# Kernel tuning notes

Hardware: AMD Instinct MI355X
Metric: run time of the kernel (lower is better)

The kernel has to match this reference:

```python
import jax, jax.numpy as jnp
import numpy as np

H = 256          # node_hidden_size (hardcoded in __init__)
NODE_EMB = 128   # node_emb_size
EDGE_EMB = 64    # edge_emb_size
L_EXTRA = 3      # num_layers - 1
NODE_FEATS = (40, 6, 5)
EDGE_FEATS = (5, 4)
T = 16           # max_seq_length
B = 32           # batch
LATENT = 128


def _lstm(inp, h, c, Wi, Wh, bi, bh):
    g = inp @ Wi + bi + h @ Wh + bh
    i, f, gg, o = jnp.split(g, 4, axis=-1)  # torch LSTMCell gate order
    c2 = jax.nn.sigmoid(f) * c + jax.nn.sigmoid(i) * jnp.tanh(gg)
    h2 = jax.nn.sigmoid(o) * jnp.tanh(c2)
    return h2, c2


def _cell(x, ctx, hs, cs, p):
    # DecoderCell: context concatenated to input of first layer, stack of LSTM cells,
    # linear projection of top hidden to emb.
    Wi0, Wh0, bi0, bh0, Wis, Whs, bis, bhs, Wout, bout = p
    inp = jnp.concatenate([x, ctx], axis=-1)
    h, c = _lstm(inp, hs[0], cs[0], Wi0, Wh0, bi0, bh0)
    nh, nc = [h], [c]
    for l in range(L_EXTRA):
        h, c = _lstm(h, hs[l + 1], cs[l + 1], Wis[l], Whs[l], bis[l], bhs[l])
        nh.append(h); nc.append(c)
    emb = h @ Wout + bout
    return emb, jnp.stack(nh), jnp.stack(nc)


def _ce(logits, tgt):
    # F.cross_entropy(..., ignore_index=-1), mean over valid batch entries
    valid = tgt >= 0
    t = jnp.where(valid, tgt, 0)
    logp = jax.nn.log_softmax(logits, axis=-1)
    nll = -jnp.take_along_axis(logp, t[:, None], axis=-1)[:, 0]
    n = jnp.sum(valid)
    return jnp.sum(jnp.where(valid, nll, 0.0)) / jnp.maximum(n, 1)


def _loss(z, latent_W, latent_b, node_p, edge_p, ncls, ecls, atom_target, bond_target):
    ctx = z @ latent_W + latent_b  # [B, H]
    NL = 1 + L_EXTRA
    hs0 = jnp.zeros((NL, B, H), jnp.float32)
    cs0 = jnp.zeros((NL, B, H), jnp.float32)
    buf0 = jnp.zeros((T, B, NODE_EMB), jnp.float32)
    x0 = jnp.zeros((B, H), jnp.float32)

    def node_step(carry, i):
        hs, cs, x, buf, loss = carry
        emb, hs2, cs2 = _cell(x, ctx, hs, cs, node_p)  # node_cell(x)
        for k, (W, b) in enumerate(ncls):
            loss = loss + _ce(emb @ W + b, atom_target[i, :, k])
        buf2 = buf.at[i].set(emb)
        ectx = cs2[-1]  # node_cell.hidden[-1][1]
        ehs0 = jnp.zeros((NL, B, H), jnp.float32)
        ecs0 = jnp.zeros((NL, B, H), jnp.float32)

        def edge_step(ec, j):
            ehs, ecs, eloss = ec
            eemb, ehs2, ecs2 = _cell(buf2[j], ectx, ehs, ecs, edge_p)
            valid = j < i  # only previous node embeddings exist; padding masked out
            ehs2 = jnp.where(valid, ehs2, ehs)
            ecs2 = jnp.where(valid, ecs2, ecs)
            for k, (W, b) in enumerate(ecls):
                eloss = eloss + _ce(eemb @ W + b, bond_target[i, :, j, k])
            return (ehs2, ecs2, eloss), None

        # reversed(node_embeddings): process j = T-1 .. 0; invalid prefix keeps zero hidden
        (ehs, ecs, eloss), _ = jax.lax.scan(
            edge_step, (ehs0, ecs0, jnp.float32(0.0)), jnp.arange(T - 1, -1, -1))
        xn = ecs[-1]  # x = edge_cell.hidden[-1][1]
        return (hs2, cs2, xn, buf2, loss + eloss), None

    init = (hs0, cs0, x0, buf0, jnp.float32(0.0))
    (hs, cs, x, buf, loss), _ = jax.lax.scan(node_step, init, jnp.arange(T))
    return loss


def setup_inputs() -> dict:
    key = jax.random.key(0)
    ks = iter(jax.random.split(key, 64))
    def rn(shape, s=0.05):
        return (jax.random.normal(next(ks), shape) * s).astype(jnp.float32)
    H4 = 4 * H
    inp = {
        'z': rn((B, LATENT), 1.0),
        'latent_W': rn((LATENT, H)), 'latent_b': rn((H,)),
        'nWi0': rn((2 * H, H4)), 'nWh0': rn((H, H4)), 'nbi0': rn((H4,)), 'nbh0': rn((H4,)),
        'nWi': rn((L_EXTRA, H, H4)), 'nWh': rn((L_EXTRA, H, H4)),
        'nbi': rn((L_EXTRA, H4)), 'nbh': rn((L_EXTRA, H4)),
        'nOutW': rn((H, NODE_EMB)), 'nOutb': rn((NODE_EMB,)),
        'eWi0': rn((NODE_EMB + H, H4)), 'eWh0': rn((H, H4)), 'ebi0': rn((H4,)), 'ebh0': rn((H4,)),
        'eWi': rn((L_EXTRA, H, H4)), 'eWh': rn((L_EXTRA, H, H4)),
        'ebi': rn((L_EXTRA, H4)), 'ebh': rn((L_EXTRA, H4)),
        'eOutW': rn((H, EDGE_EMB)), 'eOutb': rn((EDGE_EMB,)),
        'ncW0': rn((NODE_EMB, NODE_FEATS[0])), 'ncb0': rn((NODE_FEATS[0],)),
        'ncW1': rn((NODE_EMB, NODE_FEATS[1])), 'ncb1': rn((NODE_FEATS[1],)),
        'ncW2': rn((NODE_EMB, NODE_FEATS[2])), 'ncb2': rn((NODE_FEATS[2],)),
        'ecW0': rn((EDGE_EMB, EDGE_FEATS[0])), 'ecb0': rn((EDGE_FEATS[0],)),
        'ecW1': rn((EDGE_EMB, EDGE_FEATS[1])), 'ecb1': rn((EDGE_FEATS[1],)),
    }
    rng = np.random.default_rng(0)
    at = np.stack([rng.integers(0, f, size=(T, B)) for f in NODE_FEATS], axis=-1).astype(np.int32)
    bt = np.stack([rng.integers(0, f, size=(T, B, T)) for f in EDGE_FEATS], axis=-1).astype(np.int32)
    for i in range(T):
        bt[i, :, i:, :] = -1  # no edges to non-existent previous nodes (ignore_index)
    inp['atom_target'] = jnp.asarray(at)
    inp['bond_target'] = jnp.asarray(bt)
    return inp


def reference(z, atom_target, bond_target, latent_W, latent_b,
              nWi0, nWh0, nbi0, nbh0, nWi, nWh, nbi, nbh, nOutW, nOutb,
              eWi0, eWh0, ebi0, ebh0, eWi, eWh, ebi, ebh, eOutW, eOutb,
              ncW0, ncb0, ncW1, ncb1, ncW2, ncb2, ecW0, ecb0, ecW1, ecb1):
    node_p = (nWi0, nWh0, nbi0, nbh0, nWi, nWh, nbi, nbh, nOutW, nOutb)
    edge_p = (eWi0, eWh0, ebi0, ebh0, eWi, eWh, ebi, ebh, eOutW, eOutb)
    ncls = ((ncW0, ncb0), (ncW1, ncb1), (ncW2, ncb2))
    ecls = ((ecW0, ecb0), (ecW1, ecb1))
    return _loss(z, latent_W, latent_b, node_p, edge_p, ncls, ecls, atom_target, bond_target)
```

## Files before the change

### kernel.cpp

```cpp
#include <hip/hip_runtime.h>
#include <stdint.h>


#define DEVFN __device__ __forceinline__
#define SCOPE __HIP_MEMORY_SCOPE_AGENT

typedef __attribute__((ext_vector_type(8))) short bf16x8;
typedef __attribute__((ext_vector_type(4))) float f32x4;

constexpr size_t O_FLAGS = 0;
constexpr size_t O_MISC  = 16384;
constexpr size_t O_CTX   = O_MISC + 256;
constexpr size_t O_CTXG  = O_CTX + 16384;
constexpr size_t O_ZBUF  = O_CTXG + 131072;
constexpr size_t O_XBUF  = O_ZBUF + 16384;
constexpr size_t O_ECTX  = O_XBUF + 16384;
constexpr size_t O_HN    = O_ECTX + 16384;
constexpr size_t O_HE    = O_HN + 8*16384;
constexpr size_t O_EMB   = O_HE + 6*16384;
constexpr size_t O_EH3   = O_EMB + 16*8192;
constexpr size_t O_WN0   = O_EH3 + 120*16384;
constexpr size_t O_WN0C  = O_WN0 + 1024*512*2;
constexpr size_t O_WN1   = O_WN0C + 1024*256*2;
constexpr size_t O_WE0   = O_WN1 + 3*1024*512*2;
constexpr size_t O_WE1   = O_WE0 + 1024*640*2;
constexpr size_t O_NOUT  = O_WE1 + 3*1024*512*2;
constexpr size_t O_EOUT  = O_NOUT + 128*256*2;
constexpr size_t O_BN0   = O_EOUT + 64*256*2;
constexpr size_t O_BN1   = O_BN0 + 4096;
constexpr size_t O_BE0   = O_BN1 + 3*4096;
constexpr size_t O_BE1   = O_BE0 + 4096;

struct GP {
  const float *z,*lW,*lb;
  const float *nWi0,*nWh0,*nbi0,*nbh0,*nWi,*nWh,*nbi,*nbh,*nOutW,*nOutb;
  const float *eWi0,*eWh0,*ebi0,*ebh0,*eWi,*eWh,*ebi,*ebh,*eOutW,*eOutb;
  const float *ncW0,*ncb0,*ncW1,*ncb1,*ncW2,*ncb2,*ecW0,*ecb0,*ecW1,*ecb1;
  const int *atom,*bond;
  float* out; char* ws;
};

DEVFN uint16_t f2bf(float f){
  uint32_t u=__float_as_uint(f);
  uint32_t r=u+0x7fffu+((u>>16)&1u);
  return (uint16_t)(r>>16);
}
DEVFN float bf2f(uint16_t h){ return __uint_as_float(((uint32_t)h)<<16); }
DEVFN uint64_t ald64(const void* p){ return __hip_atomic_load((const uint64_t*)p,__ATOMIC_RELAXED,SCOPE); }
DEVFN uint32_t ald32(const void* p){ return __hip_atomic_load((const uint32_t*)p,__ATOMIC_RELAXED,SCOPE); }
DEVFN void ast32(void* p, uint32_t v){ __hip_atomic_store((uint32_t*)p,v,__ATOMIC_RELAXED,SCOPE); }
DEVFN float sigm(float x){ return 1.f/(1.f+__expf(-x)); }
DEVFN void acq_fence(){ __builtin_amdgcn_fence(__ATOMIC_ACQUIRE, "agent"); }

template<int K0,int K1,int K2>
DEVFN f32x4 stage_mm3(const uint16_t* p0,const uint16_t* p1,const uint16_t* p2,
                      const uint16_t* W,int rowbase,int mtile,int ntile,int lane){
  constexpr int NK=(K0+K1+K2)/32;
  const int m=lane&15, quad=lane>>4;
  const uint16_t* wrow = W + (size_t)(rowbase+ntile*16+m)*(size_t)(K0+K1+K2);
  bf16x8 aq[NK], bq[NK];
  #pragma unroll
  for(int ks=0;ks<NK;ks++){
    const int kg=ks*32;
    const uint16_t* ap; int kl;
    if (kg < K0){ ap = p0 + (size_t)(mtile*16+m)*K0; kl = kg; }
    else if (kg < K0+K1){ ap = p1 + (size_t)(mtile*16+m)*K1; kl = kg-K0; }
    else { ap = p2 + (size_t)(mtile*16+m)*K2; kl = kg-K0-K1; }
    aq[ks]=*(const bf16x8*)(ap + kl + quad*8);
    bq[ks]=*(const bf16x8*)(wrow + kg + quad*8);
  }
  f32x4 acc={0.f,0.f,0.f,0.f};
  #pragma unroll
  for(int ks=0;ks<NK;ks++)
    acc=__builtin_amdgcn_mfma_f32_16x16x32_bf16(aq[ks],bq[ks],acc,0,0,0);
  return acc;
}

DEVFN void lstm_tail(float* lds,uint16_t* hout,float& creg,bool creset,
                     uint16_t* cexp,int wgl,int tid){
  __syncthreads();
  const int b=tid>>3, ul=tid&7;
  const float* gp=&lds[b*36+ul*4];
  float gi=gp[0],gf=gp[1],gg=gp[2],go=gp[3];
  float c = creset?0.f:creg;
  float c2 = sigm(gf)*c + sigm(gi)*tanhf(gg);
  float h2 = sigm(go)*tanhf(c2);
  creg=c2;
  float hp=__shfl_xor(h2,1);
  if(!(tid&1))
    ast32(hout + b*256 + wgl*8 + ul, (uint32_t)f2bf(h2)|(((uint32_t)f2bf(hp))<<16));
  if (cexp){
    float cp=__shfl_xor(c2,1);
    if(!(tid&1))
      ast32(cexp + b*256 + wgl*8 + ul, (uint32_t)f2bf(c2)|(((uint32_t)f2bf(cp))<<16));
  }
}

DEVFN void do_lstm_r(const uint16_t* p0,const uint16_t* p1,const bf16x8* wreg,
                     const float* bvec,const float* ctxg,
                     uint16_t* hout,float& creg,bool creset,uint16_t* cexp,
                     float* lds,int wgl,int tid){
  const int lane=tid&63, wv=tid>>6, mtile=wv&1, ntile=wv>>1;
  const int m=lane&15, quad=lane>>4;
  bf16x8 aq[16];
  #pragma unroll
  for(int ks=0;ks<16;ks++){
    const uint16_t* ap = (ks<8) ? p0 + (size_t)(mtile*16+m)*256 + ks*32
                                : p1 + (size_t)(mtile*16+m)*256 + (ks-8)*32;
    aq[ks]=*(const bf16x8*)(ap + quad*8);
  }
  f32x4 acc={0.f,0.f,0.f,0.f};
  #pragma unroll
  for(int ks=0;ks<16;ks++)
    acc=__builtin_amdgcn_mfma_f32_16x16x32_bf16(aq[ks],wreg[ks],acc,0,0,0);
  const int colL=ntile*16+m, colG=wgl*32+colL;
  float bias = bvec ? bvec[colG] : 0.f;
  #pragma unroll
  for(int r=0;r<4;r++){
    int b=mtile*16+quad*4+r;
    float v=acc[r]+bias;
    if (ctxg) v += ctxg[b*1024+colG];
    lds[b*36+colL]=v;
  }
  lstm_tail(lds,hout,creg,creset,cexp,wgl,tid);
}

template<int K0,int K1,int K2>
DEVFN void do_lstm_l(const uint16_t* p0,const uint16_t* p1,const uint16_t* p2,
                     const uint16_t* slab,const float* bvec,
                     uint16_t* hout,float& creg,bool creset,uint16_t* cexp,
                     float* lds,int wgl,int tid){
  constexpr int K=K0+K1+K2, KP=K+8, NK=K/32;
  const int lane=tid&63, wv=tid>>6, mtile=wv&1, ntile=wv>>1;
  const int m=lane&15, quad=lane>>4;
  bf16x8 aq[NK];
  #pragma unroll
  for(int ks=0;ks<NK;ks++){
    const int kg=ks*32;
    const uint16_t* ap; int kl;
    if (kg < K0){ ap = p0 + (size_t)(mtile*16+m)*K0; kl = kg; }
    else if (kg < K0+K1){ ap = p1 + (size_t)(mtile*16+m)*K1; kl = kg-K0; }
    else { ap = p2 + (size_t)(mtile*16+m)*K2; kl = kg-K0-K1; }
    aq[ks]=*(const bf16x8*)(ap + kl + quad*8);
  }
  const uint16_t* wrow = slab + (size_t)(ntile*16+m)*KP;
  f32x4 acc={0.f,0.f,0.f,0.f};
  #pragma unroll
  for(int ks=0;ks<NK;ks++){
    bf16x8 bv=*(const bf16x8*)(wrow + ks*32 + quad*8);
    acc=__builtin_amdgcn_mfma_f32_16x16x32_bf16(aq[ks],bv,acc,0,0,0);
  }
  const int colL=ntile*16+m, colG=wgl*32+colL;
  float bias=bvec[colG];
  #pragma unroll
  for(int r=0;r<4;r++){
    int b=mtile*16+quad*4+r;
    lds[b*36+colL]=acc[r]+bias;
  }
  lstm_tail(lds,hout,creg,creset,cexp,wgl,tid);
}

DEVFN void do_emb(const uint16_t* h3,const uint16_t* NOUT,const float* nOutb,
                  uint16_t* dst,int wg,int tid){
  const int lane=tid&63, wv=tid>>6;
  if (wg>=8 || wv>=2) return;
  f32x4 acc=stage_mm3<256,0,0>(h3,nullptr,nullptr,NOUT,wg*16,wv,0,lane);
  const int n=lane&15, quad=lane>>4, colG=wg*16+n;
  float bias=nOutb[colG];
  #pragma unroll
  for(int r=0;r<4;r++){
    int b=wv*16+quad*4+r;
    float v=acc[r]+bias;
    float vp=__shfl_xor(v,1);
    if(!(lane&1))
      ast32(dst + b*128 + colG, (uint32_t)f2bf(v)|(((uint32_t)f2bf(vp))<<16));
  }
}

DEVFN void node_ce(const GP& P,const uint16_t* emb,int i,float* sm,float& lsum,int tid){
  {
    int e=tid*16;
    const uint64_t* src=(const uint64_t*)(emb+e);
    int b=e>>7, k=e&127;
    #pragma unroll
    for(int q=0;q<4;q++){
      uint64_t w=ald64(src+q);
      #pragma unroll
      for(int x=0;x<4;x++) sm[b*132+k+q*4+x]=bf2f((uint16_t)(w>>(16*x)));
    }
  }
  __syncthreads();
  float* ll = sm + 4224;
  const float* Ws[3]={P.ncW0,P.ncW1,P.ncW2};
  const float* bs[3]={P.ncb0,P.ncb1,P.ncb2};
  const int NCs[3]={40,6,5};
  for(int h=0;h<3;h++){
    const int Nc=NCs[h]; const float* W=Ws[h]; const float* bb=bs[h];
    for(int idx=tid; idx<32*Nc; idx+=256){
      int b=idx/Nc, c=idx-b*Nc;
      float a=bb[c];
      for(int k=0;k<128;k++) a += sm[b*132+k]*W[k*Nc+c];
      ll[b*44+c]=a;
    }
    __syncthreads();
    if (tid<32){
      int b=tid; float mx=-1e30f;
      for(int c=0;c<Nc;c++) mx=fmaxf(mx,ll[b*44+c]);
      float se=0.f;
      for(int c=0;c<Nc;c++) se+=__expf(ll[b*44+c]-mx);
      float lse=mx+__logf(se);
      int tgt=P.atom[(i*32+b)*3+h];
      lsum += (lse - ll[b*44+tgt])*(1.0f/32.0f);
    }
    __syncthreads();
  }
}

DEVFN void edge_ce(const GP& P,const uint16_t* eh3,const uint16_t* EOUT,
                   int i,int j,float* sm,float& lsum,int tid){
  const int lane=tid&63, wv=tid>>6;
  float* el=sm; float* ll=sm+4224;
  #pragma unroll
  for(int t2=0;t2<2;t2++){
    int id=wv+4*t2, mtile=id>>2, ntile=id&3;
    f32x4 acc=stage_mm3<256,0,0>(eh3,nullptr,nullptr,EOUT,0,mtile,ntile,lane);
    int n=lane&15, quad=lane>>4, colG=ntile*16+n;
    float bias=P.eOutb[colG];
    #pragma unroll
    for(int r=0;r<4;r++){ int b=mtile*16+quad*4+r; el[b*68+colG]=acc[r]+bias; }
  }
  __syncthreads();
  const float* Ws[2]={P.ecW0,P.ecW1};
  const float* bs[2]={P.ecb0,P.ecb1};
  const int NCs[2]={5,4};
  for(int h=0;h<2;h++){
    const int Nc=NCs[h]; const float* W=Ws[h];
    for(int idx=tid; idx<32*Nc; idx+=256){
      int b=idx/Nc, c=idx-b*Nc;
      float a=bs[h][c];
      for(int k=0;k<64;k++) a += el[b*68+k]*W[k*Nc+c];
      ll[b*44+c]=a;
    }
    __syncthreads();
    if (tid<32){
      int b=tid; float mx=-1e30f;
      for(int c=0;c<Nc;c++) mx=fmaxf(mx,ll[b*44+c]);
      float se=0.f;
      for(int c=0;c<Nc;c++) se+=__expf(ll[b*44+c]-mx);
      float lse=mx+__logf(se);
      int tgt=P.bond[((i*32+b)*16+j)*2+h];
      lsum += (lse - ll[b*44+tgt])*(1.0f/32.0f);
    }
    __syncthreads();
  }
}

DEVFN void wg_spin(const uint32_t* flags,int s,int lane){
  const uint32_t* f1 = flags + (size_t)lane*32;
  const uint32_t* f2 = flags + (size_t)(lane+64)*32;
  while(true){
    uint32_t a=__hip_atomic_load(f1,__ATOMIC_RELAXED,SCOPE);
    uint32_t b=__hip_atomic_load(f2,__ATOMIC_RELAXED,SCOPE);
    if (__all(((int)a>=s) && ((int)b>=s))) break;
    __builtin_amdgcn_s_sleep(1);
  }
}

__global__ __launch_bounds__(256,1) void gen_prep(GP P){
  char* ws=P.ws;
  const int tid=threadIdx.x, wg=blockIdx.x, nwg=gridDim.x;
  if (wg==0){
    for(int n=tid;n<1024;n+=256){
      int col=(n&3)*256+(n>>2);
      ((float*)(ws+O_BN0))[n]=P.nbi0[col]+P.nbh0[col];
      ((float*)(ws+O_BE0))[n]=P.ebi0[col]+P.ebh0[col];
      for(int l=0;l<3;l++){
        ((float*)(ws+O_BN1))[l*1024+n]=P.nbi[l*1024+col]+P.nbh[l*1024+col];
        ((float*)(ws+O_BE1))[l*1024+n]=P.ebi[l*1024+col]+P.ebh[l*1024+col];
      }
    }
  } else if (wg==1){
    uint16_t* ctx=(uint16_t*)(ws+O_CTX);
    for(int idx=tid; idx<8192; idx+=256){
      int b=idx>>8, n=idx&255;
      float a=P.lb[n];
      for(int k=0;k<128;k++) a += P.z[b*128+k]*P.lW[k*256+n];
      ctx[idx]=f2bf(a);
    }
  } else if (wg==2){
    uint32_t* f=(uint32_t*)(ws+O_FLAGS);
    for(int idx=tid; idx<4096; idx+=256) f[idx]=0;
    if (tid<64) ((uint32_t*)(ws+O_MISC))[tid]=0;
  } else if (wg==3){
    uint32_t* zz=(uint32_t*)(ws+O_ZBUF);
    for(int idx=tid; idx<8192; idx+=256) zz[idx]=0;
  }
  const int ROWS=9408;
  int per=(ROWS+nwg-1)/nwg;
  int r0=wg*per, r1=(r0+per<ROWS)?(r0+per):ROWS;
  for(int r=r0;r<r1;r++){
    if (r<1024){
      int n=r, col=(n&3)*256+(n>>2);
      uint16_t* dst=(uint16_t*)(ws+O_WN0)+(size_t)n*512;
      for(int k=tid;k<512;k+=256)
        dst[k]=f2bf(k<256 ? P.nWi0[k*1024+col] : P.nWh0[(k-256)*1024+col]);
    } else if (r<2048){
      int n=r-1024, col=(n&3)*256+(n>>2);
      uint16_t* dst=(uint16_t*)(ws+O_WN0C)+(size_t)n*256;
      for(int k=tid;k<256;k+=256) dst[k]=f2bf(P.nWi0[(256+k)*1024+col]);
    } else if (r<5120){
      int t=r-2048, l=t>>10, n=t&1023, col=(n&3)*256+(n>>2);
      uint16_t* dst=(uint16_t*)(ws+O_WN1)+((size_t)l*1024+n)*512;
      for(int k=tid;k<512;k+=256)
        dst[k]=f2bf(k<256 ? P.nWi[(l*256+k)*1024+col] : P.nWh[(l*256+k-256)*1024+col]);
    } else if (r<6144){
      int n=r-5120, col=(n&3)*256+(n>>2);
      uint16_t* dst=(uint16_t*)(ws+O_WE0)+(size_t)n*640;
      for(int k=tid;k<640;k+=256)
        dst[k]=f2bf(k<384 ? P.eWi0[k*1024+col] : P.eWh0[(k-384)*1024+col]);
    } else if (r<9216){
      int t=r-6144, l=t>>10, n=t&1023, col=(n&3)*256+(n>>2);
      uint16_t* dst=(uint16_t*)(ws+O_WE1)+((size_t)l*1024+n)*512;
      for(int k=tid;k<512;k+=256)
        dst[k]=f2bf(k<256 ? P.eWi[(l*256+k)*1024+col] : P.eWh[(l*256+k-256)*1024+col]);
    } else if (r<9344){
      int n=r-9216;
      uint16_t* dst=(uint16_t*)(ws+O_NOUT)+(size_t)n*256;
      for(int k=tid;k<256;k+=256) dst[k]=f2bf(P.nOutW[k*128+n]);
    } else {
      int n=r-9344;
      uint16_t* dst=(uint16_t*)(ws+O_EOUT)+(size_t)n*256;
      for(int k=tid;k<256;k+=256) dst[k]=f2bf(P.eOutW[k*64+n]);
    }
  }
}

__global__ __launch_bounds__(256,1) void gen_main(GP P){
  __shared__ alignas(16) char smem[46080];
  char* ws=P.ws;
  uint32_t* flags=(uint32_t*)(ws+O_FLAGS);
  const int tid=threadIdx.x, wg=blockIdx.x, lane=tid&63;

  if (wg<128){
    uint16_t* slab=(uint16_t*)smem;
    float* gates=(float*)(smem+41472);
    uint16_t* WN0 =(uint16_t*)(ws+O_WN0);
    uint16_t* WN0C=(uint16_t*)(ws+O_WN0C);
    uint16_t* WN1 =(uint16_t*)(ws+O_WN1);
    uint16_t* NOUT=(uint16_t*)(ws+O_NOUT);
    const float* BN0 =(const float*)(ws+O_BN0);
    const float* BN1v=(const float*)(ws+O_BN1);
    const float* BE0v=(const float*)(ws+O_BE0);
    const float* BE1v=(const float*)(ws+O_BE1);
    float* ctxg=(float*)(ws+O_CTXG);
    uint16_t* xb=(uint16_t*)(ws+O_XBUF);
    uint16_t* ec=(uint16_t*)(ws+O_ECTX);
    const uint16_t* zb=(const uint16_t*)(ws+O_ZBUF);
    uint16_t* embw=(uint16_t*)(ws+O_EMB);
    uint16_t* eh3w=(uint16_t*)(ws+O_EH3);
    auto HN=[&](int l,int pp){ return (uint16_t*)(ws+O_HN)+(size_t)(l*2+pp)*8192; };
    auto HE=[&](int l,int pp){ return (uint16_t*)(ws+O_HE)+(size_t)(l*2+pp)*8192; };

    const int g=wg>>5, wgl=wg&31;

    {
      const int KW=(g==0)?640:512, CH=KW/8, KP=KW+8;
      const uint16_t* wsrc = (g==0)
        ? (const uint16_t*)(ws+O_WE0) + (size_t)(wgl*32)*640
        : (const uint16_t*)(ws+O_WE1) + ((size_t)((g-1)*1024 + wgl*32))*512;
      for(int c=tid; c<32*CH; c+=256){
        int r=c/CH, off=c-r*CH;
        *(uint4*)(slab + (size_t)r*KP + off*8) = *(const uint4*)(wsrc + (size_t)r*KW + off*8);
      }
    }
    bf16x8 wn[16];
    {
      const uint16_t* nsrc = (g==0) ? WN0 : WN1 + (size_t)(g-1)*1024*512;
      const int m=lane&15, quad=lane>>4, ntile=(tid>>6)>>1;
      const size_t row=(size_t)(wgl*32 + ntile*16 + m);
      #pragma unroll
      for(int ks=0;ks<16;ks++)
        wn[ks]=*(const bf16x8*)(nsrc + row*512 + ks*32 + quad*8);
    }

    auto bar=[&](int sv){
      __syncthreads();
      if (tid==0) ast32(flags+(size_t)wg*32,(uint32_t)sv);
      if (tid<64){ acq_fence(); wg_spin(flags,sv,lane); }
      __syncthreads();
    };

    int s=0;
    if (g==0){
      const int wv=tid>>6, mtile=wv&1, ntile=wv>>1;
      f32x4 acc=stage_mm3<256,0,0>((const uint16_t*)(ws+O_CTX),nullptr,nullptr,
                                   WN0C,wgl*32,mtile,ntile,lane);
      const int n=lane&15, quad=lane>>4, colG=wgl*32+ntile*16+n;
      float bias=BN0[colG];
      #pragma unroll
      for(int r=0;r<4;r++){
        int b=mtile*16+quad*4+r;
        ast32(&ctxg[b*1024+colG], __float_as_uint(acc[r]+bias));
      }
    }
    bar(++s);

    float cn=0.f;
    float ce=0.f;
    for(int i=0;i<16;i++){
      const int p=i&1;
      if (g==0) do_lstm_r(xb, i?HN(0,p^1):zb, wn, nullptr, ctxg,
                          HN(0,p), cn, i==0, nullptr, gates, wgl, tid);
      bar(++s);
      if (g==1) do_lstm_r(HN(0,p), i?HN(1,p^1):zb, wn, BN1v, nullptr,
                          HN(1,p), cn, i==0, nullptr, gates, wgl, tid);
      bar(++s);
      if (g==2) do_lstm_r(HN(1,p), i?HN(2,p^1):zb, wn, BN1v+1024, nullptr,
                          HN(2,p), cn, i==0, nullptr, gates, wgl, tid);
      bar(++s);
      if (g==3) do_lstm_r(HN(2,p), i?HN(3,p^1):zb, wn, BN1v+2048, nullptr,
                          HN(3,p), cn, i==0, ec, gates, wgl, tid);
      bar(++s);
      const int nslots=(i==0)?1:(i+3);
      for(int t=0;t<nslots;t++){
        if (g==1 && t==0){
          if (wgl<8) do_emb(HN(3,p), NOUT, P.nOutb, embw+(size_t)i*4096, wgl, tid);
        } else {
          const int q=t-g;
          if (q>=0 && q<=i-1){
            const int e=q&1, j=i-1-q, pos=(i*(i-1))/2+q;
            if (g==0)
              do_lstm_l<128,256,256>(embw+(size_t)j*4096, ec, q?HE(0,e^1):zb,
                                     slab, BE0v, HE(0,e), ce, q==0, nullptr, gates, wgl, tid);
            else if (g==1)
              do_lstm_l<256,256,0>(HE(0,e), q?HE(1,e^1):zb, nullptr,
                                   slab, BE1v, HE(1,e), ce, q==0, nullptr, gates, wgl, tid);
            else if (g==2)
              do_lstm_l<256,256,0>(HE(1,e), q?HE(2,e^1):zb, nullptr,
                                   slab, BE1v+1024, HE(2,e), ce, q==0, nullptr, gates, wgl, tid);
            else
              do_lstm_l<256,256,0>(HE(2,e), q?(eh3w+(size_t)(pos-1)*8192):zb, nullptr,
                                   slab, BE1v+2048, eh3w+(size_t)pos*8192, ce, q==0,
                                   (j==0)?xb:nullptr, gates, wgl, tid);
          }
        }
        bar(++s);
      }
    }
    if (wg==0 && tid==0){
      const uint32_t* dp=(const uint32_t*)(ws+O_MISC+4);
      while (__hip_atomic_load(dp,__ATOMIC_RELAXED,SCOPE) < 8u)
        __builtin_amdgcn_s_sleep(8);
      P.out[0]=__uint_as_float(ald32(ws+O_MISC));
    }
  } else {
    float* sm=(float*)smem;
    const int my=wg-128;
    float lsum=0.f;
    int task=0, sb=1;
    const uint16_t* embw=(const uint16_t*)(ws+O_EMB);
    const uint16_t* eh3w=(const uint16_t*)(ws+O_EH3);
    const uint16_t* EOUT=(const uint16_t*)(ws+O_EOUT);
    for(int i=0;i<16;i++){
      const int base=sb+4;
      if ((task++&7)==my){
        if (tid<64) wg_spin(flags, base+1, lane);
        __syncthreads();
        acq_fence();
        node_ce(P, embw+(size_t)i*4096, i, sm, lsum, tid);
      }
      for(int j=i-1;j>=0;j--){
        const int q=i-1-j;
        if ((task++&7)==my){
          if (tid<64) wg_spin(flags, base+q+4, lane);
          __syncthreads();
          acq_fence();
          const int pos=(i*(i-1))/2+q;
          edge_ce(P, eh3w+(size_t)pos*8192, EOUT, i, j, sm, lsum, tid);
        }
      }
      sb = base + ((i==0)?1:(i+3));
    }
    #pragma unroll
    for(int off=32;off;off>>=1) lsum += __shfl_down(lsum,off);
    __syncthreads();
    if ((tid&63)==0) sm[tid>>6]=lsum;
    __syncthreads();
    if (tid==0){
      float tt=sm[0]+sm[1]+sm[2]+sm[3];
      atomicAdd((float*)(ws+O_MISC), tt);
      __threadfence();
      atomicAdd((unsigned int*)(ws+O_MISC+4), 1u);
    }
  }
}

extern "C" void kernel_launch(void* const* d_in, const int* in_sizes, int n_in,
                              void* d_out, int out_size, void* d_ws, size_t ws_size,
                              hipStream_t stream){
  (void)in_sizes; (void)n_in; (void)out_size; (void)ws_size;
  GP P;
  P.z   =(const float*)d_in[0];  P.lW  =(const float*)d_in[1];  P.lb  =(const float*)d_in[2];
  P.nWi0=(const float*)d_in[3];  P.nWh0=(const float*)d_in[4];
  P.nbi0=(const float*)d_in[5];  P.nbh0=(const float*)d_in[6];
  P.nWi =(const float*)d_in[7];  P.nWh =(const float*)d_in[8];
  P.nbi =(const float*)d_in[9];  P.nbh =(const float*)d_in[10];
  P.nOutW=(const float*)d_in[11]; P.nOutb=(const float*)d_in[12];
  P.eWi0=(const float*)d_in[13]; P.eWh0=(const float*)d_in[14];
  P.ebi0=(const float*)d_in[15]; P.ebh0=(const float*)d_in[16];
  P.eWi =(const float*)d_in[17]; P.eWh =(const float*)d_in[18];
  P.ebi =(const float*)d_in[19]; P.ebh =(const float*)d_in[20];
  P.eOutW=(const float*)d_in[21]; P.eOutb=(const float*)d_in[22];
  P.ncW0=(const float*)d_in[23]; P.ncb0=(const float*)d_in[24];
  P.ncW1=(const float*)d_in[25]; P.ncb1=(const float*)d_in[26];
  P.ncW2=(const float*)d_in[27]; P.ncb2=(const float*)d_in[28];
  P.ecW0=(const float*)d_in[29]; P.ecb0=(const float*)d_in[30];
  P.ecW1=(const float*)d_in[31]; P.ecb1=(const float*)d_in[32];
  P.atom=(const int*)d_in[33];   P.bond=(const int*)d_in[34];
  P.out=(float*)d_out; P.ws=(char*)d_ws;
  hipLaunchKernelGGL(gen_prep, dim3(120), dim3(256), 0, stream, P);
  hipLaunchKernelGGL(gen_main, dim3(136), dim3(256), 0, stream, P);
}
```

Baseline: 1.173 ms.

## Tile weight conversion through LDS transpose with coalesced loads and stores

The prep kernel's per-row weight conversion, which read fp32 weights with strided column accesses, is replaced by 64x64 tiles. Each tile is read with coalesced float4 loads, converted to bf16, transposed through shared memory and written as 16-byte vector stores. The latent-context matmul is split across four workgroups instead of one, and the prep grid is doubled. This targets the uncoalesced global traffic and serial ctx computation in the one-time weight preparation, at the cost of two barriers per tile and more complex index mapping.

After: 1.058 ms (median of 2 runs). 9.8% less time.

```diff
diff --git a/kernel.cpp b/kernel.cpp
--- a/kernel.cpp
+++ b/kernel.cpp
@@ -266,7 +266,46 @@
   }
 }
 
+DEVFN void tile_desc(const GP& P, char* ws, int tile,
+                     uint16_t*& dst,int& L,int& koff,const float*& src,
+                     int& sstr,int& N0,bool& perm){
+  if (tile<1120){
+    perm=true; sstr=1024;
+    int kt=tile>>4; N0=(tile&15)*64;
+    if (kt<4){ dst=(uint16_t*)(ws+O_WN0); L=512; koff=kt*64;
+               src=P.nWi0 + (size_t)kt*64*1024; }
+    else if (kt<8){ int r=kt-4; dst=(uint16_t*)(ws+O_WN0); L=512; koff=256+r*64;
+               src=P.nWh0 + (size_t)r*64*1024; }
+    else if (kt<12){ int r=kt-8; dst=(uint16_t*)(ws+O_WN0C); L=256; koff=r*64;
+               src=P.nWi0 + (size_t)(256+r*64)*1024; }
+    else if (kt<24){ int t=kt-12,l=t>>2,r=t&3;
+               dst=(uint16_t*)(ws+O_WN1)+(size_t)l*1024*512; L=512; koff=r*64;
+               src=P.nWi + (size_t)(l*256+r*64)*1024; }
+    else if (kt<36){ int t=kt-24,l=t>>2,r=t&3;
+               dst=(uint16_t*)(ws+O_WN1)+(size_t)l*1024*512; L=512; koff=256+r*64;
+               src=P.nWh + (size_t)(l*256+r*64)*1024; }
+    else if (kt<42){ int r=kt-36; dst=(uint16_t*)(ws+O_WE0); L=640; koff=r*64;
+               src=P.eWi0 + (size_t)r*64*1024; }
+    else if (kt<46){ int r=kt-42; dst=(uint16_t*)(ws+O_WE0); L=640; koff=384+r*64;
+               src=P.eWh0 + (size_t)r*64*1024; }
+    else if (kt<58){ int t=kt-46,l=t>>2,r=t&3;
+               dst=(uint16_t*)(ws+O_WE1)+(size_t)l*1024*512; L=512; koff=r*64;
+               src=P.eWi + (size_t)(l*256+r*64)*1024; }
+    else { int t=kt-58,l=t>>2,r=t&3;
+               dst=(uint16_t*)(ws+O_WE1)+(size_t)l*1024*512; L=512; koff=256+r*64;
+               src=P.eWh + (size_t)(l*256+r*64)*1024; }
+  } else {
+    perm=false;
+    int t2=tile-1120;
+    if (t2<8){ int r=t2>>1; N0=(t2&1)*64; dst=(uint16_t*)(ws+O_NOUT); L=256;
+               koff=r*64; src=P.nOutW + (size_t)r*64*128; sstr=128; }
+    else { int r=t2-8; N0=0; dst=(uint16_t*)(ws+O_EOUT); L=256;
+               koff=r*64; src=P.eOutW + (size_t)r*64*64; sstr=64; }
+  }
+}
+
 __global__ __launch_bounds__(256,1) void gen_prep(GP P){
+  __shared__ uint16_t tlds[64*72];
   char* ws=P.ws;
   const int tid=threadIdx.x, wg=blockIdx.x, nwg=gridDim.x;
   if (wg==0){
@@ -280,58 +319,54 @@
       }
     }
   } else if (wg==1){
+    uint32_t* f=(uint32_t*)(ws+O_FLAGS);
+    for(int idx=tid; idx<4096; idx+=256) f[idx]=0;
+    if (tid<64) ((uint32_t*)(ws+O_MISC))[tid]=0;
+  } else if (wg==2){
+    uint32_t* zz=(uint32_t*)(ws+O_ZBUF);
+    for(int idx=tid; idx<8192; idx+=256) zz[idx]=0;
+  } else if (wg>=3 && wg<7){
     uint16_t* ctx=(uint16_t*)(ws+O_CTX);
-    for(int idx=tid; idx<8192; idx+=256){
+    int i0=(wg-3)*2048;
+    for(int idx=i0+tid; idx<i0+2048; idx+=256){
       int b=idx>>8, n=idx&255;
       float a=P.lb[n];
       for(int k=0;k<128;k++) a += P.z[b*128+k]*P.lW[k*256+n];
       ctx[idx]=f2bf(a);
     }
-  } else if (wg==2){
-    uint32_t* f=(uint32_t*)(ws+O_FLAGS);
-    for(int idx=tid; idx<4096; idx+=256) f[idx]=0;
-    if (tid<64) ((uint32_t*)(ws+O_MISC))[tid]=0;
-  } else if (wg==3){
-    uint32_t* zz=(uint32_t*)(ws+O_ZBUF);
-    for(int idx=tid; idx<8192; idx+=256) zz[idx]=0;
-  }
-  const int ROWS=9408;
-  int per=(ROWS+nwg-1)/nwg;
-  int r0=wg*per, r1=(r0+per<ROWS)?(r0+per):ROWS;
-  for(int r=r0;r<r1;r++){
-    if (r<1024){
-      int n=r, col=(n&3)*256+(n>>2);
-      uint16_t* dst=(uint16_t*)(ws+O_WN0)+(size_t)n*512;
-      for(int k=tid;k<512;k+=256)
-        dst[k]=f2bf(k<256 ? P.nWi0[k*1024+col] : P.nWh0[(k-256)*1024+col]);
-    } else if (r<2048){
-      int n=r-1024, col=(n&3)*256+(n>>2);
-      uint16_t* dst=(uint16_t*)(ws+O_WN0C)+(size_t)n*256;
-      for(int k=tid;k<256;k+=256) dst[k]=f2bf(P.nWi0[(256+k)*1024+col]);
-    } else if (r<5120){
-      int t=r-2048, l=t>>10, n=t&1023, col=(n&3)*256+(n>>2);
-      uint16_t* dst=(uint16_t*)(ws+O_WN1)+((size_t)l*1024+n)*512;
-      for(int k=tid;k<512;k+=256)
-        dst[k]=f2bf(k<256 ? P.nWi[(l*256+k)*1024+col] : P.nWh[(l*256+k-256)*1024+col]);
-    } else if (r<6144){
-      int n=r-5120, col=(n&3)*256+(n>>2);
-      uint16_t* dst=(uint16_t*)(ws+O_WE0)+(size_t)n*640;
-      for(int k=tid;k<640;k+=256)
-        dst[k]=f2bf(k<384 ? P.eWi0[k*1024+col] : P.eWh0[(k-384)*1024+col]);
-    } else if (r<9216){
-      int t=r-6144, l=t>>10, n=t&1023, col=(n&3)*256+(n>>2);
-      uint16_t* dst=(uint16_t*)(ws+O_WE1)+((size_t)l*1024+n)*512;
-      for(int k=tid;k<512;k+=256)
-        dst[k]=f2bf(k<256 ? P.eWi[(l*256+k)*1024+col] : P.eWh[(l*256+k-256)*1024+col]);
-    } else if (r<9344){
-      int n=r-9216;
-      uint16_t* dst=(uint16_t*)(ws+O_NOUT)+(size_t)n*256;
-      for(int k=tid;k<256;k+=256) dst[k]=f2bf(P.nOutW[k*128+n]);
+  }
+  for(int tile=wg; tile<1132; tile+=nwg){
+    uint16_t* dst; const float* src; int L,koff,sstr,N0; bool perm;
+    tile_desc(P,ws,tile,dst,L,koff,src,sstr,N0,perm);
+    const int kq=tid>>2, q=tid&3;
+    if (perm){
+      const float* sp = src + (size_t)kq*1024 + q*256 + (N0>>2);
+      #pragma unroll
+      for(int t4=0;t4<4;t4++){
+        float4 v=*(const float4*)(sp + t4*4);
+        tlds[(q+4*(t4*4+0))*72 + kq]=f2bf(v.x);
+        tlds[(q+4*(t4*4+1))*72 + kq]=f2bf(v.y);
+        tlds[(q+4*(t4*4+2))*72 + kq]=f2bf(v.z);
+        tlds[(q+4*(t4*4+3))*72 + kq]=f2bf(v.w);
+      }
     } else {
-      int n=r-9344;
-      uint16_t* dst=(uint16_t*)(ws+O_EOUT)+(size_t)n*256;
-      for(int k=tid;k<256;k+=256) dst[k]=f2bf(P.eOutW[k*64+n]);
-    }
+      const float* sp = src + (size_t)kq*sstr + N0 + q*16;
+      #pragma unroll
+      for(int t4=0;t4<4;t4++){
+        float4 v=*(const float4*)(sp + t4*4);
+        tlds[(q*16+t4*4+0)*72 + kq]=f2bf(v.x);
+        tlds[(q*16+t4*4+1)*72 + kq]=f2bf(v.y);
+        tlds[(q*16+t4*4+2)*72 + kq]=f2bf(v.z);
+        tlds[(q*16+t4*4+3)*72 + kq]=f2bf(v.w);
+      }
+    }
+    __syncthreads();
+    const int j=tid>>2, c=tid&3;
+    uint16_t* dp = dst + (size_t)(N0+j)*L + koff + c*16;
+    const uint16_t* lp = &tlds[j*72 + c*16];
+    *(uint4*)dp       = *(const uint4*)lp;
+    *(uint4*)(dp+8)   = *(const uint4*)(lp+8);
+    __syncthreads();
   }
 }
 
@@ -518,6 +553,6 @@
   P.ecW1=(const float*)d_in[31]; P.ecb1=(const float*)d_in[32];
   P.atom=(const int*)d_in[33];   P.bond=(const int*)d_in[34];
   P.out=(float*)d_out; P.ws=(char*)d_ws;
-  hipLaunchKernelGGL(gen_prep, dim3(120), dim3(256), 0, stream, P);
+  hipLaunchKernelGGL(gen_prep, dim3(240), dim3(256), 0, stream, P);
   hipLaunchKernelGGL(gen_main, dim3(136), dim3(256), 0, stream, P);
 }
```
